# Optimization experiments

Hardware: AMD Instinct MI355X
Metric: run time of the kernel (lower is better)

Reference implementation:

```python
import jax, jax.numpy as jnp
import numpy as np

B, S, E, D = 8, 2048, 1024, 512

def setup_inputs() -> dict:
    key = jax.random.key(0)
    ks = jax.random.split(key, 7)
    scale = 1.0 / np.sqrt(E)
    return {
        "X": jax.random.normal(ks[0], (B, S, E), dtype=jnp.float32),
        "lam": jnp.float32(0.8),
        "W_q": jax.random.uniform(ks[1], (E, 2 * D), jnp.float32, -scale, scale),
        "b_q": jax.random.uniform(ks[2], (2 * D,), jnp.float32, -scale, scale),
        "W_k": jax.random.uniform(ks[3], (E, 2 * D), jnp.float32, -scale, scale),
        "b_k": jax.random.uniform(ks[4], (2 * D,), jnp.float32, -scale, scale),
        "W_v": jax.random.uniform(ks[5], (E, D), jnp.float32, -scale, scale),
        "b_v": jax.random.uniform(ks[6], (D,), jnp.float32, -scale, scale),
    }

def reference(X, lam, W_q, b_q, W_k, b_k, W_v, b_v):
    # Projections
    Q = X @ W_q + b_q          # [B, S, 2D]
    K = X @ W_k + b_k          # [B, S, 2D]
    V = X @ W_v + b_v          # [B, S, D]
    Q1, Q2 = Q[..., :D], Q[..., D:]
    K1, K2 = K[..., :D], K[..., D:]
    s = 1.0 / np.sqrt(D)
    A1 = jnp.einsum('bqd,bkd->bqk', Q1, K1) * s  # [B, S, S]
    A2 = jnp.einsum('bqd,bkd->bqk', Q2, K2) * s
    P = jax.nn.softmax(A1, axis=-1) - lam * jax.nn.softmax(A2, axis=-1)
    return jnp.einsum('bqk,bkd->bqd', P, V)      # [B, S, D]
```

## Files before the change

kernel.cpp:

```cpp
#include <hip/hip_runtime.h>


typedef unsigned short u16;
typedef short    bf16x8 __attribute__((ext_vector_type(8)));
typedef unsigned short u16x8 __attribute__((ext_vector_type(8)));
typedef unsigned short u16x4 __attribute__((ext_vector_type(4)));
typedef float    f32x4  __attribute__((ext_vector_type(4)));

typedef __attribute__((address_space(3))) unsigned int       lds_uint;
typedef __attribute__((address_space(1))) const unsigned int gl_uint;

__device__ __forceinline__ void glds16(const void* g, void* l) {
  __builtin_amdgcn_global_load_lds((gl_uint*)g, (lds_uint*)l, 16, 0, 0);
}

__device__ __forceinline__ u16 to_bf16(float f) {
  unsigned u = __float_as_uint(f);
  return (u16)((u + 0x7FFFu + ((u >> 16) & 1u)) >> 16);
}
__device__ __forceinline__ float b2f(u16 h) {
  return __uint_as_float(((unsigned)h) << 16);
}


__global__ void cvt_x(const float4* __restrict__ in, u16x4* __restrict__ out, int n4) {
  int i = blockIdx.x * 256 + threadIdx.x;
  if (i >= n4) return;
  float4 v = in[i];
  u16x4 o;
  o[0] = to_bf16(v.x); o[1] = to_bf16(v.y); o[2] = to_bf16(v.z); o[3] = to_bf16(v.w);
  out[i] = o;
}

__global__ void transpose_cvt(const float* __restrict__ in, u16* __restrict__ out,
                              int R, int C) {
  __shared__ float t[64][65];
  int c0 = blockIdx.x * 64, r0 = blockIdx.y * 64;
  int tx = threadIdx.x, ty = threadIdx.y;
  #pragma unroll
  for (int i = 0; i < 64; i += 4)
    t[ty + i][tx] = in[(long)(r0 + ty + i) * C + c0 + tx];
  __syncthreads();
  #pragma unroll
  for (int i = 0; i < 64; i += 4)
    out[(long)(c0 + ty + i) * R + r0 + tx] = to_bf16(t[tx][ty + i]);
}

__global__ void concat2(const float* __restrict__ a, const float* __restrict__ b,
                        float* __restrict__ o, int n) {
  int i = blockIdx.x * 256 + threadIdx.x;
  if (i < n) o[i] = a[i];
  else if (i < 2 * n) o[i] = b[i - n];
}

__device__ __forceinline__ void swizzle_tiles(int& tm, int& tn) {
  int nx = gridDim.x;
  int lin = blockIdx.y * nx + blockIdx.x;
  int span = nx * 4;
  int group = lin / span;
  int ing = lin % span;
  tm = group * 4 + (ing & 3);
  tn = ing >> 2;
}

__global__ __launch_bounds__(256, 4) void gemm_nt(
    const u16* __restrict__ A, int lda,
    const u16* __restrict__ B, int ldb,
    u16* __restrict__ C1, u16* __restrict__ C2, int splitN, int ldc,
    int Kd, float scale,
    const float* __restrict__ bias, int biasMode)
{
  __shared__ u16 SM[2][8192];
  u16* As = SM[0];
  u16* Bs = SM[1];

  int tid = threadIdx.x;
  int wave = tid >> 6, lane = tid & 63;
  int quad = lane >> 4, ln = lane & 15;
  int wm = wave >> 1, wn = wave & 1;
  int tm, tn;
  swizzle_tiles(tm, tn);
  int c8 = lane >> 3, ml = lane & 7;

  const f32x4 fz = {0.f, 0.f, 0.f, 0.f};
  f32x4 acc[4][4];
  #pragma unroll
  for (int i = 0; i < 4; i++)
    #pragma unroll
    for (int j = 0; j < 4; j++) acc[i][j] = fz;

  const u16* Abase = A + (long)(tm * 128 + ml) * lda + c8 * 8;
  const u16* Bbase = B + (long)(tn * 128 + ml) * ldb + c8 * 8;

  for (int kt = 0; kt < Kd; kt += 64) {
    __syncthreads();
    #pragma unroll
    for (int i = 0; i < 4; i++) {
      int mg = wave * 4 + i;
      glds16(Abase + (long)mg * 8 * lda + kt, &As[mg * 512]);
      glds16(Bbase + (long)mg * 8 * ldb + kt, &Bs[mg * 512]);
    }
    __syncthreads();
    #pragma unroll
    for (int ks = 0; ks < 2; ks++) {
      bf16x8 af[4], bfr[4];
      int c = ks * 4 + quad;
      #pragma unroll
      for (int mt = 0; mt < 4; mt++) {
        int m = wm * 64 + mt * 16 + ln;
        af[mt] = *(const bf16x8*)&As[((m >> 3) * 64 + c * 8 + (m & 7)) * 8];
      }
      #pragma unroll
      for (int nt = 0; nt < 4; nt++) {
        int n = wn * 64 + nt * 16 + ln;
        bfr[nt] = *(const bf16x8*)&Bs[((n >> 3) * 64 + c * 8 + (n & 7)) * 8];
      }
      #pragma unroll
      for (int mt = 0; mt < 4; mt++)
        #pragma unroll
        for (int nt = 0; nt < 4; nt++)
          acc[mt][nt] = __builtin_amdgcn_mfma_f32_16x16x32_bf16(af[mt], bfr[nt], acc[mt][nt], 0, 0, 0);
    }
  }

  int rowBase = tm * 128 + wm * 64;
  int colBase = tn * 128 + wn * 64;
  u16* Cw = C1; int outCol = colBase;
  if (colBase >= splitN) { Cw = C2; outCol = colBase - splitN; }
  u16* eb = &SM[0][0] + wave * 4096;

  __syncthreads();
  #pragma unroll
  for (int mt = 0; mt < 4; mt++) {
    #pragma unroll
    for (int nt = 0; nt < 4; nt++) {
      int colL = nt * 16 + ln;
      float bcol = (biasMode == 1) ? bias[colBase + colL] : 0.f;
      #pragma unroll
      for (int r = 0; r < 4; r++) {
        int rowL = mt * 16 + quad * 4 + r;
        float brow = (biasMode == 2) ? bias[rowBase + rowL] : 0.f;
        float v = acc[mt][nt][r] * scale + bcol + brow;
        eb[rowL * 64 + (((colL >> 3) ^ (rowL & 7)) << 3) + (colL & 7)] = to_bf16(v);
      }
    }
  }
  {
    int row = lane;
    long gr = (long)(rowBase + row) * ldc + outCol;
    #pragma unroll
    for (int c = 0; c < 8; c++) {
      u16x8 ch = *(const u16x8*)&eb[row * 64 + ((c ^ (row & 7)) << 3)];
      *(u16x8*)&Cw[gr + c * 8] = ch;
    }
  }
}

__device__ __forceinline__ void gemm256_core(
    const u16* __restrict__ A, int lda,
    const u16* __restrict__ B, int ldb,
    int NT, int tm, int tn, u16* SMp, f32x4 (&acc)[8][4])
{
  int tid = threadIdx.x;
  int wave = tid >> 6, lane = tid & 63;
  int quad = lane >> 4, ln = lane & 15;
  int wm = wave >> 2, wn = wave & 3;
  int c8 = lane >> 3, ml = lane & 7;

  const f32x4 fz = {0.f, 0.f, 0.f, 0.f};
  #pragma unroll
  for (int i = 0; i < 8; i++)
    #pragma unroll
    for (int j = 0; j < 4; j++) acc[i][j] = fz;

  const u16* Ab = A + (long)(tm * 256 + ml) * lda + c8 * 8;
  const u16* Bb = B + (long)(tn * 256 + ml) * ldb + c8 * 8;

  #pragma unroll
  for (int h = 0; h < 2; h++) {
    int hg = h * 16 + wave * 2;
    glds16(Ab + (long)(hg * 8) * lda,       SMp + hg * 512);
    glds16(Ab + (long)(hg * 8 + 8) * lda,   SMp + (hg + 1) * 512);
  }
  #pragma unroll
  for (int h = 0; h < 2; h++) {
    int hg = h * 16 + wave * 2;
    glds16(Bb + (long)(hg * 8) * ldb,       SMp + 2 * 16384 + hg * 512);
    glds16(Bb + (long)(hg * 8 + 8) * ldb,   SMp + 2 * 16384 + (hg + 1) * 512);
  }
  {
    int kt1 = (NT > 1) ? 64 : 0;
    #pragma unroll
    for (int h = 0; h < 2; h++) {
      int hg = h * 16 + wave * 2;
      glds16(Bb + (long)(hg * 8) * ldb + kt1,     SMp + 3 * 16384 + hg * 512);
      glds16(Bb + (long)(hg * 8 + 8) * ldb + kt1, SMp + 3 * 16384 + (hg + 1) * 512);
    }
  }
  asm volatile("s_waitcnt vmcnt(4)" ::: "memory");
  __builtin_amdgcn_s_barrier();
  __builtin_amdgcn_sched_barrier(0);

  for (int t = 0; t < NT; t++) {
    const int p = t & 1;
    const u16* Ar = SMp + p * 16384;
    const u16* Br = SMp + (2 + p) * 16384;
    bf16x8 bfr[2][4];

    #pragma unroll
    for (int q = 0; q < 4; q++) {
      bf16x8 af[2][2];
      #pragma unroll
      for (int dm = 0; dm < 2; dm++) {
        int m = wm * 128 + (q * 2 + dm) * 16 + ln;
        #pragma unroll
        for (int ks = 0; ks < 2; ks++)
          af[dm][ks] = *(const bf16x8*)(Ar + ((m >> 3) * 64 + (ks * 4 + quad) * 8 + (m & 7)) * 8);
      }
      if (q == 0) {
        #pragma unroll
        for (int nt = 0; nt < 4; nt++) {
          int n = wn * 64 + nt * 16 + ln;
          #pragma unroll
          for (int ks = 0; ks < 2; ks++)
            bfr[ks][nt] = *(const bf16x8*)(Br + ((n >> 3) * 64 + (ks * 4 + quad) * 8 + (n & 7)) * 8);
        }
      }
      if (q < 2) {
        int ktA = ((t + 1 < NT) ? (t + 1) : (NT - 1)) << 6;
        int hg = q * 16 + wave * 2;
        u16* dst = SMp + ((t + 1) & 1) * 16384;
        glds16(Ab + (long)(hg * 8) * lda + ktA,     dst + hg * 512);
        glds16(Ab + (long)(hg * 8 + 8) * lda + ktA, dst + (hg + 1) * 512);
      } else {
        int ktB = ((t + 2 < NT) ? (t + 2) : (NT - 1)) << 6;
        int hg = (q - 2) * 16 + wave * 2;
        u16* dst = SMp + (2 + p) * 16384;
        glds16(Bb + (long)(hg * 8) * ldb + ktB,     dst + hg * 512);
        glds16(Bb + (long)(hg * 8 + 8) * ldb + ktB, dst + (hg + 1) * 512);
      }
      __builtin_amdgcn_sched_barrier(0);
      __builtin_amdgcn_s_barrier();
      asm volatile("s_waitcnt lgkmcnt(0)" ::: "memory");
      __builtin_amdgcn_sched_barrier(0);
      __builtin_amdgcn_s_setprio(1);
      #pragma unroll
      for (int ks = 0; ks < 2; ks++)
        #pragma unroll
        for (int dm = 0; dm < 2; dm++)
          #pragma unroll
          for (int nt = 0; nt < 4; nt++)
            acc[q * 2 + dm][nt] = __builtin_amdgcn_mfma_f32_16x16x32_bf16(
                af[dm][ks], bfr[ks][nt], acc[q * 2 + dm][nt], 0, 0, 0);
      __builtin_amdgcn_s_setprio(0);
      __builtin_amdgcn_sched_barrier(0);
      if (q == 3) asm volatile("s_waitcnt vmcnt(4)" ::: "memory");
      __builtin_amdgcn_s_barrier();
      __builtin_amdgcn_sched_barrier(0);
    }
  }
}

__global__ __launch_bounds__(512, 2) void gemm_nt256(
    const u16* __restrict__ A, int lda,
    const u16* __restrict__ B, int ldb,
    u16* __restrict__ C1, u16* __restrict__ C2, int splitN, int ldc,
    int Kd, float scale,
    const float* __restrict__ bias, int biasMode)
{
  __shared__ u16 SM[4][16384];
  int tm, tn;
  swizzle_tiles(tm, tn);
  f32x4 acc[8][4];
  gemm256_core(A, lda, B, ldb, Kd >> 6, tm, tn, &SM[0][0], acc);

  int tid = threadIdx.x;
  int wave = tid >> 6, lane = tid & 63;
  int quad = lane >> 4, ln = lane & 15;
  int wm = wave >> 2, wn = wave & 3;

  int rowBase = tm * 256 + wm * 128;
  int colBase = tn * 256 + wn * 64;
  u16* Cw = C1; int outCol = colBase;
  if (colBase >= splitN) { Cw = C2; outCol = colBase - splitN; }
  u16* eb = &SM[0][0] + wave * 8192;

  asm volatile("s_waitcnt vmcnt(0)" ::: "memory");
  __builtin_amdgcn_s_barrier();
  __builtin_amdgcn_sched_barrier(0);

  #pragma unroll
  for (int mt = 0; mt < 8; mt++) {
    #pragma unroll
    for (int nt = 0; nt < 4; nt++) {
      int colL = nt * 16 + ln;
      float bcol = (biasMode == 1) ? bias[colBase + colL] : 0.f;
      #pragma unroll
      for (int r = 0; r < 4; r++) {
        int rowL = mt * 16 + quad * 4 + r;
        float brow = (biasMode == 2) ? bias[rowBase + rowL] : 0.f;
        float v = acc[mt][nt][r] * scale + bcol + brow;
        eb[rowL * 64 + (((colL >> 3) ^ (rowL & 7)) << 3) + (colL & 7)] = to_bf16(v);
      }
    }
  }
  #pragma unroll
  for (int rr = 0; rr < 2; rr++) {
    int row = rr * 64 + lane;
    long gr = (long)(rowBase + row) * ldc + outCol;
    #pragma unroll
    for (int c = 0; c < 8; c++) {
      u16x8 ch = *(const u16x8*)&eb[row * 64 + ((c ^ (row & 7)) << 3)];
      *(u16x8*)&Cw[gr + c * 8] = ch;
    }
  }
}

__global__ __launch_bounds__(512, 2) void gemm_s256(
    const u16* __restrict__ Q, const u16* __restrict__ K,
    u16* __restrict__ E1, u16* __restrict__ E2,
    float* __restrict__ statsP, float scale)
{
  __shared__ u16 SM[4][16384];
  int bz = blockIdx.z >> 1, half = blockIdx.z & 1;
  const u16* A = Q + (long)bz * 2097152 + half * 512;
  const u16* B = K + (long)bz * 2097152 + half * 512;
  u16* Ed = (half ? E2 : E1) + (long)bz * 4194304;
  statsP += (long)blockIdx.z * 65536;

  int tm, tn;
  swizzle_tiles(tm, tn);
  f32x4 acc[8][4];
  gemm256_core(A, 1024, B, 1024, 8 , tm, tn, &SM[0][0], acc);

  int tid = threadIdx.x;
  int wave = tid >> 6, lane = tid & 63;
  int quad = lane >> 4, ln = lane & 15;
  int wm = wave >> 2, wn = wave & 3;

  int rowBase = tm * 256 + wm * 128;
  int colBase = tn * 256 + wn * 64;
  int kb = tn * 4 + wn;
  u16* eb = &SM[0][0] + wave * 8192;

  asm volatile("s_waitcnt vmcnt(0)" ::: "memory");
  __builtin_amdgcn_s_barrier();
  __builtin_amdgcn_sched_barrier(0);

  #pragma unroll
  for (int mt = 0; mt < 8; mt++) {
    #pragma unroll
    for (int nt = 0; nt < 4; nt++) {
      int colL = nt * 16 + ln;
      #pragma unroll
      for (int r = 0; r < 4; r++) {
        int rowL = mt * 16 + quad * 4 + r;
        eb[rowL * 64 + (((colL >> 3) ^ (rowL & 7)) << 3) + (colL & 7)] =
            to_bf16(__expf(acc[mt][nt][r] * scale));
      }
    }
  }
  #pragma unroll
  for (int rr = 0; rr < 2; rr++) {
    int row = rr * 64 + lane;
    u16x8 ch[8];
    #pragma unroll
    for (int c = 0; c < 8; c++)
      ch[c] = *(const u16x8*)&eb[row * 64 + ((c ^ (row & 7)) << 3)];
    u16* Ep = Ed + (long)(rowBase + row) * 2048 + colBase;
    #pragma unroll
    for (int c = 0; c < 8; c++)
      *(u16x8*)&Ep[c * 8] = ch[c];
    float L = 0.f;
    #pragma unroll
    for (int c = 0; c < 8; c++)
      #pragma unroll
      for (int j = 0; j < 8; j++) L += b2f(ch[c][j]);
    statsP[(rowBase + row) * 32 + kb] = L;
  }
}

__global__ void stats_reduce(const float* __restrict__ sp, float* __restrict__ so,
                             const float* __restrict__ lamPtr) {
  int gid = blockIdx.x * 256 + threadIdx.x;
  const float* p = sp + (long)gid * 32;
  float L = 0.f;
  #pragma unroll
  for (int kb = 0; kb < 32; kb++) L += p[kb];
  int half = (gid >> 11) & 1;
  so[gid] = (half ? lamPtr[0] : 1.0f) / L;
}

__global__ __launch_bounds__(256, 4) void apply_pv(
    const u16* __restrict__ E1, const u16* __restrict__ E2,
    const u16* __restrict__ VT, const float* __restrict__ inv,
    float* __restrict__ Out)
{
  __shared__ u16 Ps[32 * 72];
  __shared__ u16 Vs[512 * 64];
  __shared__ float i1s[32], i2s[32];

  int b = blockIdx.x & 7, qt = blockIdx.x >> 3;
  int q0 = qt * 32;
  int tid = threadIdx.x;
  int wave = tid >> 6, lane = tid & 63, quad = lane >> 4, ln = lane & 15;

  if (tid < 32) {
    i1s[tid] = inv[(long)(b * 2 + 0) * 2048 + q0 + tid];
  } else if (tid < 64) {
    int r = tid - 32;
    i2s[r] = inv[(long)(b * 2 + 1) * 2048 + q0 + r];
  }

  const f32x4 fz = {0.f, 0.f, 0.f, 0.f};
  f32x4 acc[2][8];
  #pragma unroll
  for (int mt = 0; mt < 2; mt++)
    #pragma unroll
    for (int nt = 0; nt < 8; nt++) acc[mt][nt] = fz;

  int d0 = wave * 128;
  int c8 = lane >> 3, ml = lane & 7;
  int r = tid >> 3, cg = (tid & 7) * 8;
  const u16* e1p = E1 + ((long)b * 2048 + q0 + r) * 2048 + cg;
  const u16* e2p = E2 + ((long)b * 2048 + q0 + r) * 2048 + cg;
  float i1 = 0.f, i2 = 0.f;

  u16x8 a1 = *(const u16x8*)(e1p);
  u16x8 a2 = *(const u16x8*)(e2p);

  for (int kt = 0; kt < 2048; kt += 64) {
    __syncthreads();
    #pragma unroll
    for (int i = 0; i < 16; i++) {
      int dg = wave * 16 + i;
      glds16(VT + (long)(dg * 8 + ml) * 16384 + b * 2048 + kt + c8 * 8, &Vs[dg * 512]);
    }
    if (kt == 0) { i1 = i1s[r]; i2 = i2s[r]; }
    u16x8 o1;
    #pragma unroll
    for (int j = 0; j < 8; j++)
      o1[j] = to_bf16(b2f(a1[j]) * i1 - b2f(a2[j]) * i2);
    *(u16x8*)&Ps[r * 72 + cg] = o1;
    if (kt + 64 < 2048) {
      a1 = *(const u16x8*)(e1p + kt + 64);
      a2 = *(const u16x8*)(e2p + kt + 64);
    }
    __syncthreads();

    #pragma unroll
    for (int ks = 0; ks < 2; ks++) {
      bf16x8 pf[2], vf[8];
      int c = ks * 4 + quad;
      #pragma unroll
      for (int mt = 0; mt < 2; mt++)
        pf[mt] = *(const bf16x8*)&Ps[(mt * 16 + ln) * 72 + ks * 32 + quad * 8];
      #pragma unroll
      for (int nt = 0; nt < 8; nt++) {
        int d = d0 + nt * 16 + ln;
        vf[nt] = *(const bf16x8*)&Vs[((d >> 3) * 64 + c * 8 + (d & 7)) * 8];
      }
      #pragma unroll
      for (int mt = 0; mt < 2; mt++)
        #pragma unroll
        for (int nt = 0; nt < 8; nt++)
          acc[mt][nt] = __builtin_amdgcn_mfma_f32_16x16x32_bf16(pf[mt], vf[nt], acc[mt][nt], 0, 0, 0);
    }
  }

  #pragma unroll
  for (int mt = 0; mt < 2; mt++)
    #pragma unroll
    for (int nt = 0; nt < 8; nt++)
      #pragma unroll
      for (int r2 = 0; r2 < 4; r2++)
        Out[((long)b * 2048 + q0 + mt * 16 + quad * 4 + r2) * 512 + d0 + nt * 16 + ln] =
            acc[mt][nt][r2];
}


extern "C" void kernel_launch(void* const* d_in, const int* in_sizes, int n_in,
                              void* d_out, int out_size, void* d_ws, size_t ws_size,
                              hipStream_t stream)
{
  const float* X   = (const float*)d_in[0];
  const float* lam = (const float*)d_in[1];
  const float* Wq  = (const float*)d_in[2];
  const float* bq  = (const float*)d_in[3];
  const float* Wk  = (const float*)d_in[4];
  const float* bk  = (const float*)d_in[5];
  const float* Wv  = (const float*)d_in[6];
  const float* bv  = (const float*)d_in[7];
  float* Out = (float*)d_out;
  char* ws = (char*)d_ws;

  u16*  WqkT   = (u16*)(ws + 0);
  u16*  WvT    = (u16*)(ws + 4194304);
  float* bqk   = (float*)(ws + 5242880);
  u16*  Qb     = (u16*)(ws + 6291456);
  u16*  Kb     = (u16*)(ws + 39845888);
  u16*  VTb    = (u16*)(ws + 73400320);
  u16*  Xb     = (u16*)(ws + 90177536);
  u16*  E1     = (u16*)(ws + 90177536);
  u16*  E2     = (u16*)(ws + 157286400);
  float* statsP= (float*)(ws + 224395264);
  float* invD  = (float*)(ws + 228589568);

  cvt_x<<<16384, 256, 0, stream>>>((const float4*)X, (u16x4*)Xb, 4194304);
  transpose_cvt<<<dim3(16, 16), dim3(64, 4), 0, stream>>>(Wq, WqkT, 1024, 1024);
  transpose_cvt<<<dim3(16, 16), dim3(64, 4), 0, stream>>>(Wk, WqkT + 1024 * 1024, 1024, 1024);
  transpose_cvt<<<dim3(8, 16),  dim3(64, 4), 0, stream>>>(Wv, WvT, 1024, 512);
  concat2<<<8, 256, 0, stream>>>(bq, bk, bqk, 1024);

  gemm_nt256<<<dim3(8, 64), 512, 0, stream>>>(Xb, 1024, WqkT, 1024,
                                              Qb, Kb, 1024, 1024,
                                              1024, 1.0f, bqk, 1);
  gemm_nt<<<dim3(128, 4), 256, 0, stream>>>(WvT, 1024, Xb, 1024,
                                            VTb, VTb, 1 << 30, 16384,
                                            1024, 1.0f, bv, 2);

  const float s = 0.044194173824159216f;
  gemm_s256<<<dim3(8, 8, 16), 512, 0, stream>>>(Qb, Kb, E1, E2, statsP, s);

  stats_reduce<<<128, 256, 0, stream>>>(statsP, invD, lam);
  apply_pv<<<512, 256, 0, stream>>>(E1, E2, VTb, invD, Out);
}
```

Before: 544.1 us.

## Double-buffer V and P tiles in apply_pv with 64-row blocks

Rewrites the P·V kernel to use 512-thread blocks covering 64 query rows, doubling the reuse of each V tile loaded into LDS. V and P are double-buffered in LDS, so global-to-LDS loads and the next P tile's combine are interleaved with the MFMA work through explicit waitcnt, barriers and setprio. This targets exposed load latency and halves the total V traffic. The cost is a large LDS footprint (about 144KB) and half as many blocks, which may reduce occupancy on the GPU.

```diff
diff --git a/kernel.cpp b/kernel.cpp
--- a/kernel.cpp
+++ b/kernel.cpp
@@ -391,90 +391,133 @@
   so[gid] = (half ? lamPtr[0] : 1.0f) / L;
 }
 
-__global__ __launch_bounds__(256, 4) void apply_pv(
+__global__ __launch_bounds__(512, 2) void apply_pv(
     const u16* __restrict__ E1, const u16* __restrict__ E2,
     const u16* __restrict__ VT, const float* __restrict__ inv,
     float* __restrict__ Out)
 {
-  __shared__ u16 Ps[32 * 72];
-  __shared__ u16 Vs[512 * 64];
-  __shared__ float i1s[32], i2s[32];
-
+  __shared__ u16 Vs[2][32768];
+  __shared__ u16 Pb[2][4096];
+  __shared__ float i1s[64], i2s[64];
+
+  const int NT = 32;
   int b = blockIdx.x & 7, qt = blockIdx.x >> 3;
-  int q0 = qt * 32;
+  int q0 = qt * 64;
   int tid = threadIdx.x;
   int wave = tid >> 6, lane = tid & 63, quad = lane >> 4, ln = lane & 15;
-
-  if (tid < 32) {
-    i1s[tid] = inv[(long)(b * 2 + 0) * 2048 + q0 + tid];
-  } else if (tid < 64) {
-    int r = tid - 32;
-    i2s[r] = inv[(long)(b * 2 + 1) * 2048 + q0 + r];
-  }
+  int c8 = lane >> 3, ml = lane & 7;
+  int r = tid >> 3, cg8 = tid & 7;
+
+  const u16* e1p = E1 + ((long)b * 2048 + q0 + r) * 2048 + cg8 * 8;
+  const u16* e2p = E2 + ((long)b * 2048 + q0 + r) * 2048 + cg8 * 8;
+  const u16* Vbase = VT + (long)b * 2048;
+  int pw = (r >> 3) * 512 + cg8 * 64 + (r & 7) * 8;
 
   const f32x4 fz = {0.f, 0.f, 0.f, 0.f};
-  f32x4 acc[2][8];
-  #pragma unroll
-  for (int mt = 0; mt < 2; mt++)
-    #pragma unroll
-    for (int nt = 0; nt < 8; nt++) acc[mt][nt] = fz;
-
-  int d0 = wave * 128;
-  int c8 = lane >> 3, ml = lane & 7;
-  int r = tid >> 3, cg = (tid & 7) * 8;
-  const u16* e1p = E1 + ((long)b * 2048 + q0 + r) * 2048 + cg;
-  const u16* e2p = E2 + ((long)b * 2048 + q0 + r) * 2048 + cg;
-  float i1 = 0.f, i2 = 0.f;
-
+  f32x4 acc[4][4];
+  #pragma unroll
+  for (int i = 0; i < 4; i++)
+    #pragma unroll
+    for (int j = 0; j < 4; j++) acc[i][j] = fz;
+
+  if (tid < 64)       i1s[tid]       = inv[(long)(b * 2 + 0) * 2048 + q0 + tid];
+  else if (tid < 128) i2s[tid - 64]  = inv[(long)(b * 2 + 1) * 2048 + q0 + (tid - 64)];
   u16x8 a1 = *(const u16x8*)(e1p);
   u16x8 a2 = *(const u16x8*)(e2p);
-
-  for (int kt = 0; kt < 2048; kt += 64) {
-    __syncthreads();
-    #pragma unroll
-    for (int i = 0; i < 16; i++) {
-      int dg = wave * 16 + i;
-      glds16(VT + (long)(dg * 8 + ml) * 16384 + b * 2048 + kt + c8 * 8, &Vs[dg * 512]);
-    }
-    if (kt == 0) { i1 = i1s[r]; i2 = i2s[r]; }
-    u16x8 o1;
+  __builtin_amdgcn_sched_barrier(0);
+  #pragma unroll
+  for (int i = 0; i < 8; i++) {
+    int dg = wave * 8 + i;
+    glds16(Vbase + (long)(dg * 8 + ml) * 16384 + c8 * 8, &Vs[0][dg * 512]);
+  }
+  __builtin_amdgcn_sched_barrier(0);
+  asm volatile("s_waitcnt lgkmcnt(0)" ::: "memory");
+  __builtin_amdgcn_s_barrier();
+  __builtin_amdgcn_sched_barrier(0);
+  float i1 = i1s[r], i2 = i2s[r];
+  {
+    u16x8 o;
     #pragma unroll
     for (int j = 0; j < 8; j++)
-      o1[j] = to_bf16(b2f(a1[j]) * i1 - b2f(a2[j]) * i2);
-    *(u16x8*)&Ps[r * 72 + cg] = o1;
-    if (kt + 64 < 2048) {
-      a1 = *(const u16x8*)(e1p + kt + 64);
-      a2 = *(const u16x8*)(e2p + kt + 64);
-    }
-    __syncthreads();
-
-    #pragma unroll
-    for (int ks = 0; ks < 2; ks++) {
-      bf16x8 pf[2], vf[8];
-      int c = ks * 4 + quad;
-      #pragma unroll
-      for (int mt = 0; mt < 2; mt++)
-        pf[mt] = *(const bf16x8*)&Ps[(mt * 16 + ln) * 72 + ks * 32 + quad * 8];
-      #pragma unroll
-      for (int nt = 0; nt < 8; nt++) {
-        int d = d0 + nt * 16 + ln;
-        vf[nt] = *(const bf16x8*)&Vs[((d >> 3) * 64 + c * 8 + (d & 7)) * 8];
-      }
-      #pragma unroll
-      for (int mt = 0; mt < 2; mt++)
-        #pragma unroll
-        for (int nt = 0; nt < 8; nt++)
-          acc[mt][nt] = __builtin_amdgcn_mfma_f32_16x16x32_bf16(pf[mt], vf[nt], acc[mt][nt], 0, 0, 0);
-    }
-  }
-
-  #pragma unroll
-  for (int mt = 0; mt < 2; mt++)
-    #pragma unroll
-    for (int nt = 0; nt < 8; nt++)
+      o[j] = to_bf16(b2f(a1[j]) * i1 - b2f(a2[j]) * i2);
+    *(u16x8*)&Pb[0][pw] = o;
+  }
+  a1 = *(const u16x8*)(e1p + 64);
+  a2 = *(const u16x8*)(e2p + 64);
+  __builtin_amdgcn_sched_barrier(0);
+  asm volatile("s_waitcnt lgkmcnt(0)" ::: "memory");
+  asm volatile("s_waitcnt vmcnt(2)" ::: "memory");
+  __builtin_amdgcn_sched_barrier(0);
+  __builtin_amdgcn_s_barrier();
+  __builtin_amdgcn_sched_barrier(0);
+
+  for (int t = 0; t < NT; t++) {
+    const int p = t & 1;
+    const u16* Vr = &Vs[p][0];
+    const u16* Pr = &Pb[p][0];
+    u16* Vw = &Vs[p ^ 1][0];
+    u16* Pw = &Pb[p ^ 1][0];
+    int ktv = ((t + 1 < NT) ? (t + 1) : (NT - 1)) << 6;
+    int kte = ((t + 2 < NT) ? (t + 2) : (NT - 1)) << 6;
+    bf16x8 vf[2][4];
+
+    #pragma unroll
+    for (int q = 0; q < 4; q++) {
+      bf16x8 pf[2];
+      #pragma unroll
+      for (int ks = 0; ks < 2; ks++) {
+        int m = q * 16 + ln;
+        pf[ks] = *(const bf16x8*)&Pr[((m >> 3) * 64 + (ks * 4 + quad) * 8 + (m & 7)) * 8];
+      }
+      if (q == 0) {
+        #pragma unroll
+        for (int ks = 0; ks < 2; ks++)
+          #pragma unroll
+          for (int nt = 0; nt < 4; nt++) {
+            int d = wave * 64 + nt * 16 + ln;
+            vf[ks][nt] = *(const bf16x8*)&Vr[((d >> 3) * 64 + (ks * 4 + quad) * 8 + (d & 7)) * 8];
+          }
+      }
+      #pragma unroll
+      for (int i = 0; i < 2; i++) {
+        int dg = wave * 8 + q * 2 + i;
+        glds16(Vbase + (long)(dg * 8 + ml) * 16384 + ktv + c8 * 8, Vw + dg * 512);
+      }
+      if (q == 3) {
+        __builtin_amdgcn_sched_barrier(0);
+        u16x8 o;
+        #pragma unroll
+        for (int j = 0; j < 8; j++)
+          o[j] = to_bf16(b2f(a1[j]) * i1 - b2f(a2[j]) * i2);
+        *(u16x8*)&Pw[pw] = o;
+        a1 = *(const u16x8*)(e1p + kte);
+        a2 = *(const u16x8*)(e2p + kte);
+      }
+      __builtin_amdgcn_sched_barrier(0);
+      __builtin_amdgcn_s_barrier();
+      asm volatile("s_waitcnt lgkmcnt(0)" ::: "memory");
+      __builtin_amdgcn_sched_barrier(0);
+      __builtin_amdgcn_s_setprio(1);
+      #pragma unroll
+      for (int ks = 0; ks < 2; ks++)
+        #pragma unroll
+        for (int nt = 0; nt < 4; nt++)
+          acc[q][nt] = __builtin_amdgcn_mfma_f32_16x16x32_bf16(pf[ks], vf[ks][nt], acc[q][nt], 0, 0, 0);
+      __builtin_amdgcn_s_setprio(0);
+      __builtin_amdgcn_sched_barrier(0);
+      if (q == 3) asm volatile("s_waitcnt vmcnt(2)" ::: "memory");
+      __builtin_amdgcn_s_barrier();
+      __builtin_amdgcn_sched_barrier(0);
+    }
+  }
+
+  #pragma unroll
+  for (int mt = 0; mt < 4; mt++)
+    #pragma unroll
+    for (int nt = 0; nt < 4; nt++)
       #pragma unroll
       for (int r2 = 0; r2 < 4; r2++)
-        Out[((long)b * 2048 + q0 + mt * 16 + quad * 4 + r2) * 512 + d0 + nt * 16 + ln] =
+        Out[((long)b * 2048 + q0 + mt * 16 + quad * 4 + r2) * 512 + wave * 64 + nt * 16 + ln] =
             acc[mt][nt][r2];
 }
 
@@ -523,5 +566,5 @@
   gemm_s256<<<dim3(8, 8, 16), 512, 0, stream>>>(Qb, Kb, E1, E2, statsP, s);
 
   stats_reduce<<<128, 256, 0, stream>>>(statsP, invD, lam);
-  apply_pv<<<512, 256, 0, stream>>>(E1, E2, VTb, invD, Out);
-}
+  apply_pv<<<256, 512, 0, stream>>>(E1, E2, VTb, invD, Out);
+}
```

After: 475.6 us. 12.6% less time.
